# Kernel optimization log

Measured on AMD Instinct MI355X. Metric: run time of the kernel, lower is better.

## Reference

```python
import jax, jax.numpy as jnp
import numpy as np

B, N, D = 4, 4096, 512          # batch, seq_len, hidden_size
H, DH = 8, 64                    # n_heads, head_dim
M = 512                          # nb_features = 0.125 * seq_len
LN_EPS = 1e-12
KERNEL_EPS = 1e-4


def setup_inputs() -> dict:
    key = jax.random.key(0)
    ks = jax.random.split(key, 12)
    s = 0.02
    return {
        "input_tensor": jax.random.normal(ks[0], (B, N, D), jnp.float32),
        "attention_mask": jnp.zeros((B, 1, 1, N), jnp.float32),  # unused by module
        "Wq": jax.random.normal(ks[1], (D, D), jnp.float32) * s,
        "bq": jnp.zeros((D,), jnp.float32),
        "Wk": jax.random.normal(ks[2], (D, D), jnp.float32) * s,
        "bk": jnp.zeros((D,), jnp.float32),
        "Wv": jax.random.normal(ks[3], (D, D), jnp.float32) * s,
        "bv": jnp.zeros((D,), jnp.float32),
        # gaussian (orthogonal-style) random feature projections [M, DH]
        "proj_q": jax.random.normal(ks[4], (M, DH), jnp.float32),
        "proj_k": jax.random.normal(ks[5], (M, DH), jnp.float32),
        "Wd": jax.random.normal(ks[6], (D, D), jnp.float32) * s,
        "bd": jnp.zeros((D,), jnp.float32),
        "gamma": jnp.ones((D,), jnp.float32),
        "beta": jnp.zeros((D,), jnp.float32),
    }


def _softmax_kernel(data, projection_matrix, is_query):
    # data: [B,H,N,DH], projection_matrix: [M,DH]
    data_normalizer = data.shape[-1] ** (-0.25)
    ratio = projection_matrix.shape[0] ** (-0.5)
    data_dash = jnp.einsum("bhnd,md->bhnm", data_normalizer * data, projection_matrix)
    diag_data = (jnp.sum(data * data, axis=-1) * 0.5 * data_normalizer ** 2)[..., None]
    if is_query:
        stab = jnp.max(data_dash, axis=-1, keepdims=True)
    else:
        stab = jnp.max(data_dash)  # global max, per original code
    return ratio * (jnp.exp(data_dash - diag_data - stab) + KERNEL_EPS)


def _linear_attention(q, k, v):
    # q,k: [B,H,N,M]; v: [B,H,N,DH]
    k_cumsum = jnp.sum(k, axis=-2)                               # [B,H,M]
    d_inv = 1.0 / jnp.einsum("bhnm,bhm->bhn", q, k_cumsum)       # [B,H,N]
    context = jnp.einsum("bhnm,bhne->bhme", k, v)                # [B,H,M,DH]
    return jnp.einsum("bhme,bhnm,bhn->bhne", context, q, d_inv)  # [B,H,N,DH]


def reference(input_tensor, attention_mask, Wq, bq, Wk, bk, Wv, bv,
              proj_q, proj_k, Wd, bd, gamma, beta):
    def heads(x):  # [B,N,D] -> [B,H,N,DH]
        return x.reshape(B, N, H, DH).transpose(0, 2, 1, 3)

    q = heads(input_tensor @ Wq.T + bq)
    k = heads(input_tensor @ Wk.T + bk)
    v = heads(input_tensor @ Wv.T + bv)

    q = _softmax_kernel(q, proj_q, is_query=True)
    k = _softmax_kernel(k, proj_k, is_query=False)

    ctx = _linear_attention(q, k, v)                  # [B,H,N,DH]
    ctx = ctx.transpose(0, 2, 1, 3).reshape(B, N, D)  # merge heads

    hidden = ctx @ Wd.T + bd                          # dropout is identity (eval)
    x = hidden + input_tensor
    mu = jnp.mean(x, axis=-1, keepdims=True)
    var = jnp.mean((x - mu) ** 2, axis=-1, keepdims=True)
    return (x - mu) / jnp.sqrt(var + LN_EPS) * gamma + beta
```

## Files before the change

kernel.cpp:

```cpp
#include <hip/hip_runtime.h>
#include <math.h>

typedef __bf16 bf16;
typedef __bf16 bf16x8 __attribute__((ext_vector_type(8)));
typedef __bf16 bf16x4 __attribute__((ext_vector_type(4)));
typedef float  f32x4  __attribute__((ext_vector_type(4)));

#define NSEQ 4096
#define DMODEL 512
#define DHEAD 64
#define MFEAT 512
#define BHEADS 32
#define ROWS_TOTAL 16384

#define NORMALIZER 0.35355339059327373f
#define DIAG_C 0.0625f
#define KEPS 1e-4f

__device__ __forceinline__ float warpReduceSum(float v) {
#pragma unroll
    for (int off = 32; off > 0; off >>= 1) v += __shfl_xor(v, off);
    return v;
}

// ... 97 lines not shown
                int row = (wr << 6) + (mi << 4) + (l & 15);
                int addr = ((row << 7) + (ks << 6) + ((l >> 4) << 4)) ^ ((row & 7) << 4);
                af[mi] = *(const bf16x8*)(As + addr);
            }
#pragma unroll
            for (int nj = 0; nj < 4; ++nj) {
                int row = (wc << 6) + (nj << 4) + (l & 15);
                int addr = ((row << 7) + (ks << 6) + ((l >> 4) << 4)) ^ ((row & 7) << 4);
                bb[nj] = *(const bf16x8*)(Bs + addr);
            }
#pragma unroll
            for (int mi = 0; mi < 4; ++mi)
#pragma unroll
                for (int nj = 0; nj < 4; ++nj)
                    acc[mi][nj] = __builtin_amdgcn_mfma_f32_16x16x32_bf16(af[mi], bb[nj], acc[mi][nj], 0, 0, 0);
        }
        __syncthreads();
    }

    const int subrow = (l >> 4) << 2;
    const int subcol = l & 15;
#pragma unroll
    for (int mi = 0; mi < 4; ++mi) {
#pragma unroll
        for (int nj = 0; nj < 4; ++nj) {
            const int cg = col0 + (wc << 6) + (nj << 4) + subcol;
            const float bi = bias[cg];
            const int rgb = row0 + (wr << 6) + (mi << 4) + subrow;
            if (MODE == 0) {
                if (cg < 512) {
                    const int hh = cg >> 6, ee = cg & 63;
                    const int bb2 = rgb >> 12, n = rgb & 4095;
#pragma unroll
                    for (int r = 0; r < 4; ++r)
                        outQ[((size_t)((bb2 * 8 + hh) * 4096 + n + r)) * 64 + ee] =
                            (bf16)(acc[mi][nj][r] + bi);
                } else if (cg < 1024) {
                    const int eg = cg - 512, hh = eg >> 6, ee = eg & 63;
#pragma unroll
                    for (int r = 0; r < 4; ++r) {
                        const int rg = rgb + r;
                        *(bf16*)((char*)outK + (size_t)rg * 1024 + hh * 128 +
                                 ((ee * 2) ^ ((rg & 7) << 4))) = (bf16)(acc[mi][nj][r] + bi);
                    }
                } else {
                    const int eg = cg - 1024, hh = eg >> 6, ee = eg & 63;
                    const int bb2 = rgb >> 12, n = rgb & 4095;
                    bf16x4 pv;
#pragma unroll
                    for (int r = 0; r < 4; ++r) pv[r] = (bf16)(acc[mi][nj][r] + bi);
                    const int nb = n * 2;
                    size_t byteaddr = (size_t)((bb2 * 8 + hh) * 64 + ee) * 8192
                                    + (size_t)((nb & ~127) | ((nb & 127) ^ ((ee & 7) << 4)));
                    *(bf16x4*)((char*)outV + byteaddr) = pv;
                }
            } else {
#pragma unroll
                for (int r = 0; r < 4; ++r) {
                    const int rg = rgb + r;
                    outF[(size_t)rg * 512 + cg] = acc[mi][nj][r] + bi + resid[(size_t)rg * 512 + cg];
                }
            }
        }
    }
}

__global__ __launch_bounds__(64)
void vsum_kernel(const bf16* __restrict__ Vt, float* __restrict__ vsum)
{
    const int row = blockIdx.x;
    const bf16x8* p = (const bf16x8*)((const char*)Vt + (size_t)row * 8192);
    float s = 0.f;
#pragma unroll
    for (int i = 0; i < 8; ++i) {
        bf16x8 v = p[threadIdx.x + i * 64];
#pragma unroll
        for (int u = 0; u < 8; ++u) s += (float)v[u];
    }
    s = warpReduceSum(s);
    if (threadIdx.x == 0) vsum[row] = s;
}

__global__ __launch_bounds__(256)
void kside_mfma2(const bf16* __restrict__ Kb, const bf16* __restrict__ Vt,
                 const float* __restrict__ projk,
                 float* __restrict__ ctxp4, float* __restrict__ esumf4,
                 float* __restrict__ gmax)
{
    __shared__ char K_s[16384];
    __shared__ char V_s[16384];
    __shared__ char E_s[16384];
    __shared__ float diag_s[128];
    __shared__ float part_s[4][64];
    __shared__ float wmax_s[4];

    const int tid = threadIdx.x;
    const int w = tid >> 6, l = tid & 63;
    const int bh = blockIdx.x;
    const int b = bh >> 3, h = bh & 7;
    const int m0 = blockIdx.y << 6;
    const int z = blockIdx.z;

    bf16x8 pk[4][2];
#pragma unroll
    for (int nj = 0; nj < 4; ++nj)
#pragma unroll
        for (int ks = 0; ks < 2; ++ks) {
            const int m = m0 + (nj << 4) + (l & 15);
            const int e0 = (ks << 5) + ((l >> 4) << 3);
            const float* p = projk + (size_t)m * 64 + e0;
            float4 a = *(const float4*)p;
            float4 c = *(const float4*)(p + 4);
            bf16x8 f;
            f[0] = (bf16)a.x; f[1] = (bf16)a.y; f[2] = (bf16)a.z; f[3] = (bf16)a.w;
            f[4] = (bf16)c.x; f[5] = (bf16)c.y; f[6] = (bf16)c.z; f[7] = (bf16)c.w;
            pk[nj][ks] = f;
        }

    const char* kg = (const char*)Kb + ((size_t)(b * 4096) * 512 + h * 64) * 2
                   + (size_t)((w << 3) + (l >> 3)) * 1024 + ((l & 7) << 4);
    const char* vg = (const char*)Vt + (size_t)bh * 64 * 8192
                   + (size_t)((w << 2) + (l >> 4)) * 8192 + ((l & 15) << 4);

    float esacc[4] = {0.f, 0.f, 0.f, 0.f};
    float lmax = -1e30f;
    f32x4 acc2[4] = {};

    for (int c = 0; c < 8; ++c) {
        const int n0 = (z << 10) + (c << 7);
#pragma unroll
        for (int i = 0; i < 4; ++i) {
            gload16(kg + (size_t)(n0 + (i << 5)) * 1024, K_s + (i << 12) + (w << 10));
            gload16(vg + (size_t)(i << 4) * 8192 + (n0 << 1), V_s + (i << 12) + (w << 10));
        }
        __syncthreads();

        f32x4 acc1[2][4] = {};
        float ss[2] = {0.f, 0.f};
#pragma unroll
        for (int ks = 0; ks < 2; ++ks) {
            bf16x8 af[2];
#pragma unroll
            for (int mi = 0; mi < 2; ++mi) {
                const int n = (w << 5) + (mi << 4) + (l & 15);
                const int addr = ((n << 7) + (ks << 6) + ((l >> 4) << 4)) ^ ((n & 7) << 4);
                af[mi] = *(const bf16x8*)(K_s + addr);
#pragma unroll
                for (int u = 0; u < 8; ++u) { float f = (float)af[mi][u]; ss[mi] += f * f; }
            }
#pragma unroll
            for (int mi = 0; mi < 2; ++mi)
#pragma unroll
                for (int nj = 0; nj < 4; ++nj)
                    acc1[mi][nj] = __builtin_amdgcn_mfma_f32_16x16x32_bf16(af[mi], pk[nj][ks], acc1[mi][nj], 0, 0, 0);
        }
#pragma unroll
        for (int mi = 0; mi < 2; ++mi) {
            float s = ss[mi];
            s += __shfl_xor(s, 16); s += __shfl_xor(s, 32);
            if (l < 16) diag_s[(w << 5) + (mi << 4) + l] = DIAG_C * s;
        }
#pragma unroll
        for (int mi = 0; mi < 2; ++mi) {
            const int nrow0 = (w << 5) + (mi << 4) + ((l >> 4) << 2);
#pragma unroll
            for (int nj = 0; nj < 4; ++nj) {
                const int m = (nj << 4) + (l & 15);
                bf16x4 ev;
#pragma unroll
                for (int r = 0; r < 4; ++r) {
                    float kd = NORMALIZER * acc1[mi][nj][r];
                    lmax = fmaxf(lmax, kd);
                    float e = __expf(kd - diag_s[nrow0 + r]);
                    esacc[nj] += e;
                    ev[r] = (bf16)e;
                }
                const int addr = ((m << 8) + (nrow0 << 1)) ^ ((m & 7) << 4);
                *(bf16x4*)(E_s + addr) = ev;
            }
        }
        __syncthreads();

#pragma unroll
        for (int ks = 0; ks < 4; ++ks) {
            const int mrow = (w << 4) + (l & 15);
            const int aaddr = ((mrow << 8) + (ks << 6) + ((l >> 4) << 4)) ^ ((mrow & 7) << 4);
            bf16x8 aE = *(const bf16x8*)(E_s + aaddr);
#pragma unroll
            for (int ej = 0; ej < 4; ++ej) {
                const int e = (ej << 4) + (l & 15);
                const int vaddr = ((e << 8) + (ks << 6) + ((l >> 4) << 4)) ^ ((e & 7) << 4);
                bf16x8 bV = *(const bf16x8*)(V_s + vaddr);
                acc2[ej] = __builtin_amdgcn_mfma_f32_16x16x32_bf16(aE, bV, acc2[ej], 0, 0, 0);
            }
        }
        __syncthreads();
    }

#pragma unroll
    for (int nj = 0; nj < 4; ++nj) {
        float s = esacc[nj];
        s += __shfl_xor(s, 16); s += __shfl_xor(s, 32);
        if (l < 16) part_s[w][(nj << 4) + l] = s;
    }
#pragma unroll
    for (int off = 32; off > 0; off >>= 1) lmax = fmaxf(lmax, __shfl_xor(lmax, off));
    if (l == 0) wmax_s[w] = lmax;
    __syncthreads();
    if (tid < 64) {
        float es = part_s[0][tid] + part_s[1][tid] + part_s[2][tid] + part_s[3][tid];
        esumf4[((size_t)z * 32 + bh) * 512 + m0 + tid] = es;
        if (tid == 0)
            atomicMaxF(gmax, fmaxf(fmaxf(wmax_s[0], wmax_s[1]), fmaxf(wmax_s[2], wmax_s[3])));
    }
    const size_t zbase = (size_t)z * (32 * 512 * 64);
    const int mrow0 = m0 + (w << 4) + ((l >> 4) << 2);
#pragma unroll
    for (int ej = 0; ej < 4; ++ej) {
        const int e = (ej << 4) + (l & 15);
#pragma unroll
        for (int r = 0; r < 4; ++r)
            ctxp4[zbase + ((size_t)(bh * 512 + mrow0 + r)) * 64 + e] = acc2[ej][r];
    }
}

__global__ __launch_bounds__(256)
void finalize_ctx(const float* __restrict__ ctxp4, const float* __restrict__ esumf4,
                  bf16* __restrict__ ctxE, float* __restrict__ ctxsum,
                  float* __restrict__ esumsum)
{
    __shared__ float red_s[4][64];
    const int tid = threadIdx.x;
    const int bh = blockIdx.x;
    const int m0 = blockIdx.y << 7;
    const int e = tid & 63, ms = tid >> 6;
    const size_t Z = (size_t)32 * 512 * 64;

    const float* cb = ctxp4 + ((size_t)bh * 512 + m0 + ms * 32) * 64 + e;
    char* obr = (char*)ctxE + ((size_t)bh * 80 + e) * 1024;
    float s = 0.f;
#pragma unroll
    for (int i8 = 0; i8 < 4; ++i8) {
        bf16x8 pk8;
#pragma unroll
        for (int u = 0; u < 8; ++u) {
            const size_t off = (size_t)(i8 * 8 + u) * 64;
            float v = cb[off] + cb[off + Z] + cb[off + 2 * Z] + cb[off + 3 * Z];
            s += v;
            pk8[u] = (bf16)v;
        }
        const int inrow = ((m0 + ms * 32 + i8 * 8) << 1) ^ ((e & 7) << 4);
        *(bf16x8*)(obr + inrow) = pk8;
    }
    red_s[ms][e] = s;
    __syncthreads();
    if (tid < 64)
        atomicAdd(ctxsum + bh * 64 + tid,
                  red_s[0][tid] + red_s[1][tid] + red_s[2][tid] + red_s[3][tid]);
    if (tid < 128) {
        const int m = m0 + tid;
        float ev = esumf4[(size_t)bh * 512 + m]
                 + esumf4[((size_t)32 + bh) * 512 + m]
                 + esumf4[((size_t)64 + bh) * 512 + m]
                 + esumf4[((size_t)96 + bh) * 512 + m];
        bf16* er = ctxE + (size_t)(bh * 80 + 64) * 512;
        er[m] = (bf16)1.0f;
        er[512 + (m ^ 8)] = (bf16)ev;
        float t = warpReduceSum(ev);
        if ((tid & 63) == 0) atomicAdd(esumsum + bh, t);
    }
}

__global__ __launch_bounds__(512, 1)
void qside_mfma4(const bf16* __restrict__ Qb, const bf16* __restrict__ Pq,
                 const bf16* __restrict__ CtxE, const float* __restrict__ vsum,
                 const float* __restrict__ ctxsum, const float* __restrict__ esumsum,
                 const float* __restrict__ gmax, bf16* __restrict__ OutC)
{
    __shared__ char ctx_s[81920];
    __shared__ char pq_s[2][16384];
    __shared__ char T_s[40960];

    const int tid = threadIdx.x;
    const int w = tid >> 6, l = tid & 63;
    const int lq = l & 15, lg = l >> 4;
    const int bh = blockIdx.x;
    const int b = bh >> 3, h = bh & 7;
    const int n0 = blockIdx.y << 9;

    const char* ctxg = (const char*)CtxE + (size_t)bh * 81920;
    const char* pqg  = (const char*)Pq;
#pragma unroll
    for (int i = 0; i < 10; ++i)
        gload16(ctxg + (i << 13) + (tid << 4), ctx_s + (i << 13) + (w << 10));
#pragma unroll
    for (int p = 0; p < 2; ++p)
        gload16(pqg + (p << 13) + (tid << 4), pq_s[0] + (p << 13) + (w << 10));

    const char* qgb = (const char*)Qb + ((size_t)bh * 4096 + n0 + (w << 6)) * 128;
    bf16x8 qa[4][2];
    float diag_l[4];
#pragma unroll
    for (int ni = 0; ni < 4; ++ni) {
        const char* qr = qgb + ((ni << 4) + lq) * 128;
        float ss = 0.f;
#pragma unroll
        for (int kk = 0; kk < 2; ++kk) {
            qa[ni][kk] = *(const bf16x8*)(qr + (kk << 6) + (lg << 4));
#pragma unroll
            for (int u = 0; u < 8; ++u) { float f = (float)qa[ni][kk][u]; ss += f * f; }
        }
        ss += __shfl_xor(ss, 16);
        ss += __shfl_xor(ss, 32);
        diag_l[ni] = DIAG_C * ss;
    }

    f32x4 acc2[4][5] = {};
    float mmax[4] = {-1e30f, -1e30f, -1e30f, -1e30f};
    char* tw = T_s + w * 5120;
    const f32x4 Zc = {0.f, 0.f, 0.f, 0.f};

    __syncthreads();

    for (int ft = 0; ft < 4; ++ft) {
        const int buf = ft & 1;
        if (ft < 3) {
#pragma unroll
            for (int p = 0; p < 2; ++p)
                gload16(pqg + ((ft + 1) << 14) + (p << 13) + (tid << 4),
                        pq_s[buf ^ 1] + (p << 13) + (w << 10));
        }
        const char* pqb = pq_s[buf];
#pragma unroll
        for (int sl = 0; sl < 4; ++sl) {
            f32x4 acc1[2][4];
#pragma unroll
            for (int mi = 0; mi < 2; ++mi) {
                const int fr = (sl << 5) + (mi << 4) + lq;
                bf16x8 pf = *(const bf16x8*)(pqb + fr * 128 +
                              (((lg << 4)) ^ ((lq & 7) << 4)));
#pragma unroll
                for (int ni = 0; ni < 4; ++ni)
                    acc1[mi][ni] = __builtin_amdgcn_mfma_f32_16x16x32_bf16(pf, qa[ni][0], Zc, 0, 0, 0);
            }
#pragma unroll
            for (int mi = 0; mi < 2; ++mi) {
                const int fr = (sl << 5) + (mi << 4) + lq;
// ... 47 lines not shown
            const float uT = __shfl(acc2[ni][4][r], (lg << 4));
            const float uE = __shfl(acc2[ni][4][r], (lg << 4) | 1);
            const float cr = __expf(-NORMALIZER * mm);
            const float qsum = cr * uT + KEPS * 512.0f;
            const float D = sG * (cr * uE + KEPS * ess) + KEPS * 4096.0f * qsum;
            const float inv = 1.0f / D;
            const float al = sG * cr * inv;
            const float G1 = sG * KEPS * inv;
            const float G2 = KEPS * qsum * inv;
            const int row = (ni << 4) + (lg << 2) + r;
#pragma unroll
            for (int nj = 0; nj < 4; ++nj) {
                const int e = (nj << 4) + lq;
                float v = al * acc2[ni][nj][r] + G1 * ctxsum[(bh << 6) + e] + G2 * vsum[(bh << 6) + e];
                outb[(size_t)row * 512 + e] = (bf16)v;
            }
        }
    }
}

__global__ __launch_bounds__(256)
void ln_kernel(const float* __restrict__ hid, const float* __restrict__ gamma,
               const float* __restrict__ beta, float* __restrict__ out)
{
    const int row = (blockIdx.x << 2) + (threadIdx.x >> 6);
    const int lane = threadIdx.x & 63;
    const float* x = hid + (size_t)row * DMODEL + (lane << 3);
    float4 a = *(const float4*)x;
    float4 c = *(const float4*)(x + 4);
    float s = a.x + a.y + a.z + a.w + c.x + c.y + c.z + c.w;
    float sq = a.x * a.x + a.y * a.y + a.z * a.z + a.w * a.w +
               c.x * c.x + c.y * c.y + c.z * c.z + c.w * c.w;
    s = warpReduceSum(s);
    sq = warpReduceSum(sq);
    const float mu = s * 0.001953125f;
    const float var = sq * 0.001953125f - mu * mu;
    const float rs = rsqrtf(var + 1e-12f);
    const float4 g1 = *(const float4*)(gamma + (lane << 3));
    const float4 g2 = *(const float4*)(gamma + (lane << 3) + 4);
    const float4 b1 = *(const float4*)(beta + (lane << 3));
    const float4 b2 = *(const float4*)(beta + (lane << 3) + 4);
    float4 o1, o2;
    o1.x = (a.x - mu) * rs * g1.x + b1.x;
    o1.y = (a.y - mu) * rs * g1.y + b1.y;
    o1.z = (a.z - mu) * rs * g1.z + b1.z;
    o1.w = (a.w - mu) * rs * g1.w + b1.w;
    o2.x = (c.x - mu) * rs * g2.x + b2.x;
    o2.y = (c.y - mu) * rs * g2.y + b2.y;
    o2.z = (c.z - mu) * rs * g2.z + b2.z;
    o2.w = (c.w - mu) * rs * g2.w + b2.w;
    *(float4*)(out + (size_t)row * DMODEL + (lane << 3)) = o1;
    *(float4*)(out + (size_t)row * DMODEL + (lane << 3) + 4) = o2;
}

__global__ void init_misc(float* gmax)
{
    if (threadIdx.x == 0 && blockIdx.x == 0) *gmax = -1e30f;
}

extern "C" void kernel_launch(void* const* d_in, const int* in_sizes, int n_in,
                              void* d_out, int out_size, void* d_ws, size_t ws_size,
                              hipStream_t stream)
{
    const float* x     = (const float*)d_in[0];
    const float* Wq    = (const float*)d_in[2];
    const float* bq    = (const float*)d_in[3];
    const float* Wk    = (const float*)d_in[4];
    const float* bk    = (const float*)d_in[5];
    const float* Wv    = (const float*)d_in[6];
    const float* bv    = (const float*)d_in[7];
    const float* projq = (const float*)d_in[8];
    const float* projk = (const float*)d_in[9];
    const float* Wd    = (const float*)d_in[10];
    const float* bd    = (const float*)d_in[11];
    const float* gamma = (const float*)d_in[12];
    const float* beta  = (const float*)d_in[13];

    char* W = (char*)d_ws;
    bf16*  qb16   = (bf16*) (W);
    bf16*  kb16s  = (bf16*) (W + 16777216);
    bf16*  vtb    = (bf16*) (W + 33554432);
    bf16*  xb16   = (bf16*) (W + 50331648);
    float* hidf32 = (float*)(W + 67108864);
    float* ctxp4  = (float*)(W + 67108864);
    float* esumf4 = (float*)(W + 83886080);
    bf16*  Wb16   = (bf16*) (W + 100663296);
    bf16*  Wdb16  = (bf16*) (W + 102236160);
    bf16*  pqb16  = (bf16*) (W + 102760448);
    float* bcat   = (float*)(W + 102825984);
    bf16*  ctxE   = (bf16*) (W + 102832128);
    float* vsumb  = (float*)(W + 105453568);
    float* ctxsum = (float*)(W + 105461760);
    float* esmsm  = (float*)(W + 105469952);
    float* gmaxb  = (float*)(W + 105470080);

    prep_convert<<<9250, 256, 0, stream>>>(x, Wq, Wk, Wv, Wd, projq, bq, bk, bv,
                                           xb16, Wb16, Wdb16, pqb16, bcat);
    hipMemsetAsync(ctxE, 0, 2621440, stream);
    hipMemsetAsync(ctxsum, 0, 8192 + 128, stream);
    init_misc<<<1, 64, 0, stream>>>(gmaxb);

    gemm_mfma<0><<<dim3(12, 128), 256, 0, stream>>>(xb16, Wb16, bcat, nullptr,
                                                    qb16, kb16s, vtb, nullptr);

    vsum_kernel<<<2048, 64, 0, stream>>>(vtb, vsumb);
    kside_mfma2<<<dim3(32, 8, 4), 256, 0, stream>>>(kb16s, vtb, projk,
                                                    ctxp4, esumf4, gmaxb);
    finalize_ctx<<<dim3(32, 4), 256, 0, stream>>>(ctxp4, esumf4, ctxE, ctxsum, esmsm);

    qside_mfma4<<<dim3(32, 8), 512, 0, stream>>>(qb16, pqb16, ctxE, vsumb,
                                                 ctxsum, esmsm, gmaxb, xb16);

    gemm_mfma<1><<<dim3(4, 128), 256, 0, stream>>>(xb16, Wdb16, bd, x,
                                                   nullptr, nullptr, nullptr, hidf32);
    ln_kernel<<<4096, 256, 0, stream>>>(hidf32, gamma, beta, (float*)d_out);
}
```

Measured before the change: 193.6 us.

## Widen k-side feature tile to 128 and overlap K/V loads with compute

The k-side kernel now covers 128 random features per block instead of 64, so each K/V chunk loaded into shared memory feeds twice as many MFMAs and the grid's y-dimension halves. Diagonal norms are passed between lanes with shuffles instead of going through shared memory. The next K chunk is prefetched during the E·V MFMA phase and the V load is issued right after the barrier, which removes one barrier per iteration. In exchange the block uses more registers and more LDS (E_s is doubled) and launches fewer blocks, which may lower occupancy and parallelism.

```diff
diff --git a/kernel.cpp b/kernel.cpp
--- a/kernel.cpp
+++ b/kernel.cpp
@@ -203,146 +203,177 @@
 }
 
 __global__ __launch_bounds__(256)
-void kside_mfma2(const bf16* __restrict__ Kb, const bf16* __restrict__ Vt,
+void kside_mfma3(const bf16* __restrict__ Kb, const bf16* __restrict__ Vt,
                  const float* __restrict__ projk,
                  float* __restrict__ ctxp4, float* __restrict__ esumf4,
                  float* __restrict__ gmax)
 {
     __shared__ char K_s[16384];
     __shared__ char V_s[16384];
-    __shared__ char E_s[16384];
-    __shared__ float diag_s[128];
-    __shared__ float part_s[4][64];
+    __shared__ char E_s[32768];
+    __shared__ float part_s[4][128];
     __shared__ float wmax_s[4];
 
     const int tid = threadIdx.x;
     const int w = tid >> 6, l = tid & 63;
+    const int lq = l & 15, lg = l >> 4;
     const int bh = blockIdx.x;
     const int b = bh >> 3, h = bh & 7;
-    const int m0 = blockIdx.y << 6;
+    const int M0 = blockIdx.y << 7;
     const int z = blockIdx.z;
 
-    bf16x8 pk[4][2];
-#pragma unroll
-    for (int nj = 0; nj < 4; ++nj)
-#pragma unroll
-        for (int ks = 0; ks < 2; ++ks) {
-            const int m = m0 + (nj << 4) + (l & 15);
-            const int e0 = (ks << 5) + ((l >> 4) << 3);
-            const float* p = projk + (size_t)m * 64 + e0;
-            float4 a = *(const float4*)p;
-            float4 c = *(const float4*)(p + 4);
-            bf16x8 f;
-            f[0] = (bf16)a.x; f[1] = (bf16)a.y; f[2] = (bf16)a.z; f[3] = (bf16)a.w;
-            f[4] = (bf16)c.x; f[5] = (bf16)c.y; f[6] = (bf16)c.z; f[7] = (bf16)c.w;
-            pk[nj][ks] = f;
-        }
+    bf16x8 pk[2][4][2];
+#pragma unroll
+    for (int mh = 0; mh < 2; ++mh)
+#pragma unroll
+        for (int mj = 0; mj < 4; ++mj)
+#pragma unroll
+            for (int ks = 0; ks < 2; ++ks) {
+                const int m = M0 + (mh << 6) + (mj << 4) + lq;
+                const float* p = projk + (size_t)m * 64 + (ks << 5) + (lg << 3);
+                float4 a = *(const float4*)p;
+                float4 c = *(const float4*)(p + 4);
+                bf16x8 f;
+                f[0] = (bf16)a.x; f[1] = (bf16)a.y; f[2] = (bf16)a.z; f[3] = (bf16)a.w;
+                f[4] = (bf16)c.x; f[5] = (bf16)c.y; f[6] = (bf16)c.z; f[7] = (bf16)c.w;
+                pk[mh][mj][ks] = f;
+            }
 
     const char* kg = (const char*)Kb + ((size_t)(b * 4096) * 512 + h * 64) * 2
                    + (size_t)((w << 3) + (l >> 3)) * 1024 + ((l & 7) << 4);
     const char* vg = (const char*)Vt + (size_t)bh * 64 * 8192
                    + (size_t)((w << 2) + (l >> 4)) * 8192 + ((l & 15) << 4);
 
-    float esacc[4] = {0.f, 0.f, 0.f, 0.f};
+    float esacc[2][4] = {};
     float lmax = -1e30f;
-    f32x4 acc2[4] = {};
+    f32x4 acc2[2][4] = {};
+
+    {
+        const int n0 = z << 10;
+#pragma unroll
+        for (int i = 0; i < 4; ++i)
+            gload16(kg + (size_t)(n0 + (i << 5)) * 1024, K_s + (i << 12) + (w << 10));
+    }
 
     for (int c = 0; c < 8; ++c) {
-        const int n0 = (z << 10) + (c << 7);
-#pragma unroll
-        for (int i = 0; i < 4; ++i) {
-            gload16(kg + (size_t)(n0 + (i << 5)) * 1024, K_s + (i << 12) + (w << 10));
-            gload16(vg + (size_t)(i << 4) * 8192 + (n0 << 1), V_s + (i << 12) + (w << 10));
-        }
+        const int nc = (z << 10) + (c << 7);
         __syncthreads();
-
-        f32x4 acc1[2][4] = {};
+#pragma unroll
+        for (int i = 0; i < 4; ++i)
+            gload16(vg + (size_t)(i << 4) * 8192 + (nc << 1), V_s + (i << 12) + (w << 10));
+
+        bf16x8 af[2][2];
         float ss[2] = {0.f, 0.f};
 #pragma unroll
-        for (int ks = 0; ks < 2; ++ks) {
-            bf16x8 af[2];
-#pragma unroll
-            for (int mi = 0; mi < 2; ++mi) {
-                const int n = (w << 5) + (mi << 4) + (l & 15);
-                const int addr = ((n << 7) + (ks << 6) + ((l >> 4) << 4)) ^ ((n & 7) << 4);
-                af[mi] = *(const bf16x8*)(K_s + addr);
-#pragma unroll
-                for (int u = 0; u < 8; ++u) { float f = (float)af[mi][u]; ss[mi] += f * f; }
-            }
-#pragma unroll
-            for (int mi = 0; mi < 2; ++mi)
-#pragma unroll
-                for (int nj = 0; nj < 4; ++nj)
-                    acc1[mi][nj] = __builtin_amdgcn_mfma_f32_16x16x32_bf16(af[mi], pk[nj][ks], acc1[mi][nj], 0, 0, 0);
-        }
-#pragma unroll
-        for (int mi = 0; mi < 2; ++mi) {
-            float s = ss[mi];
+        for (int ni = 0; ni < 2; ++ni) {
+            const int n = (w << 5) + (ni << 4) + lq;
+#pragma unroll
+            for (int ks = 0; ks < 2; ++ks) {
+                const int addr = ((n << 7) + (ks << 6) + (lg << 4)) ^ ((n & 7) << 4);
+                af[ni][ks] = *(const bf16x8*)(K_s + addr);
+#pragma unroll
+                for (int u = 0; u < 8; ++u) { float f = (float)af[ni][ks][u]; ss[ni] += f * f; }
+            }
+            ss[ni] += __shfl_xor(ss[ni], 16);
+            ss[ni] += __shfl_xor(ss[ni], 32);
+        }
+        float dgc[2][4];
+#pragma unroll
+        for (int ni = 0; ni < 2; ++ni)
+#pragma unroll
+            for (int r = 0; r < 4; ++r)
+                dgc[ni][r] = DIAG_C * __shfl(ss[ni], (lg << 2) + r);
+
+#pragma unroll
+        for (int mh = 0; mh < 2; ++mh) {
+            f32x4 acc1[2][4] = {};
+#pragma unroll
+            for (int ks = 0; ks < 2; ++ks)
+#pragma unroll
+                for (int ni = 0; ni < 2; ++ni)
+#pragma unroll
+                    for (int mj = 0; mj < 4; ++mj)
+                        acc1[ni][mj] = __builtin_amdgcn_mfma_f32_16x16x32_bf16(
+                            af[ni][ks], pk[mh][mj][ks], acc1[ni][mj], 0, 0, 0);
+#pragma unroll
+            for (int ni = 0; ni < 2; ++ni) {
+                const int nl0 = (w << 5) + (ni << 4) + (lg << 2);
+#pragma unroll
+                for (int mj = 0; mj < 4; ++mj) {
+                    const int mloc = (mh << 6) + (mj << 4) + lq;
+                    bf16x4 ev;
+#pragma unroll
+                    for (int r = 0; r < 4; ++r) {
+                        float kd = NORMALIZER * acc1[ni][mj][r];
+                        lmax = fmaxf(lmax, kd);
+                        float e = __expf(kd - dgc[ni][r]);
+                        esacc[mh][mj] += e;
+                        ev[r] = (bf16)e;
+                    }
+                    const int addr = ((mloc << 8) + (nl0 << 1)) ^ ((mloc & 7) << 4);
+                    *(bf16x4*)(E_s + addr) = ev;
+                }
+            }
+        }
+        __syncthreads();
+        if (c < 7) {
+            const int nn = (z << 10) + ((c + 1) << 7);
+#pragma unroll
+            for (int i = 0; i < 4; ++i)
+                gload16(kg + (size_t)(nn + (i << 5)) * 1024, K_s + (i << 12) + (w << 10));
+        }
+#pragma unroll
+        for (int ks = 0; ks < 4; ++ks) {
+            bf16x8 ae[2];
+#pragma unroll
+            for (int mj2 = 0; mj2 < 2; ++mj2) {
+                const int mloc = (w << 5) + (mj2 << 4) + lq;
+                const int addr = ((mloc << 8) + (ks << 6) + (lg << 4)) ^ ((mloc & 7) << 4);
+                ae[mj2] = *(const bf16x8*)(E_s + addr);
+            }
+#pragma unroll
+            for (int ej = 0; ej < 4; ++ej) {
+                const int e = (ej << 4) + lq;
+                const int vaddr = ((e << 8) + (ks << 6) + (lg << 4)) ^ ((e & 7) << 4);
+                bf16x8 bV = *(const bf16x8*)(V_s + vaddr);
+#pragma unroll
+                for (int mj2 = 0; mj2 < 2; ++mj2)
+                    acc2[mj2][ej] = __builtin_amdgcn_mfma_f32_16x16x32_bf16(
+                        ae[mj2], bV, acc2[mj2][ej], 0, 0, 0);
+            }
+        }
+    }
+
+#pragma unroll
+    for (int mh = 0; mh < 2; ++mh)
+#pragma unroll
+        for (int mj = 0; mj < 4; ++mj) {
+            float s = esacc[mh][mj];
             s += __shfl_xor(s, 16); s += __shfl_xor(s, 32);
-            if (l < 16) diag_s[(w << 5) + (mi << 4) + l] = DIAG_C * s;
-        }
-#pragma unroll
-        for (int mi = 0; mi < 2; ++mi) {
-            const int nrow0 = (w << 5) + (mi << 4) + ((l >> 4) << 2);
-#pragma unroll
-            for (int nj = 0; nj < 4; ++nj) {
-                const int m = (nj << 4) + (l & 15);
-                bf16x4 ev;
-#pragma unroll
-                for (int r = 0; r < 4; ++r) {
-                    float kd = NORMALIZER * acc1[mi][nj][r];
-                    lmax = fmaxf(lmax, kd);
-                    float e = __expf(kd - diag_s[nrow0 + r]);
-                    esacc[nj] += e;
-                    ev[r] = (bf16)e;
-                }
-                const int addr = ((m << 8) + (nrow0 << 1)) ^ ((m & 7) << 4);
-                *(bf16x4*)(E_s + addr) = ev;
-            }
-        }
-        __syncthreads();
-
-#pragma unroll
-        for (int ks = 0; ks < 4; ++ks) {
-            const int mrow = (w << 4) + (l & 15);
-            const int aaddr = ((mrow << 8) + (ks << 6) + ((l >> 4) << 4)) ^ ((mrow & 7) << 4);
-            bf16x8 aE = *(const bf16x8*)(E_s + aaddr);
-#pragma unroll
-            for (int ej = 0; ej < 4; ++ej) {
-                const int e = (ej << 4) + (l & 15);
-                const int vaddr = ((e << 8) + (ks << 6) + ((l >> 4) << 4)) ^ ((e & 7) << 4);
-                bf16x8 bV = *(const bf16x8*)(V_s + vaddr);
-                acc2[ej] = __builtin_amdgcn_mfma_f32_16x16x32_bf16(aE, bV, acc2[ej], 0, 0, 0);
-            }
-        }
-        __syncthreads();
-    }
-
-#pragma unroll
-    for (int nj = 0; nj < 4; ++nj) {
-        float s = esacc[nj];
-        s += __shfl_xor(s, 16); s += __shfl_xor(s, 32);
-        if (l < 16) part_s[w][(nj << 4) + l] = s;
-    }
+            if (l < 16) part_s[w][(mh << 6) + (mj << 4) + l] = s;
+        }
 #pragma unroll
     for (int off = 32; off > 0; off >>= 1) lmax = fmaxf(lmax, __shfl_xor(lmax, off));
     if (l == 0) wmax_s[w] = lmax;
     __syncthreads();
-    if (tid < 64) {
+    if (tid < 128) {
         float es = part_s[0][tid] + part_s[1][tid] + part_s[2][tid] + part_s[3][tid];
-        esumf4[((size_t)z * 32 + bh) * 512 + m0 + tid] = es;
-        if (tid == 0)
-            atomicMaxF(gmax, fmaxf(fmaxf(wmax_s[0], wmax_s[1]), fmaxf(wmax_s[2], wmax_s[3])));
-    }
+        esumf4[((size_t)z * 32 + bh) * 512 + M0 + tid] = es;
+    }
+    if (tid == 0)
+        atomicMaxF(gmax, fmaxf(fmaxf(wmax_s[0], wmax_s[1]), fmaxf(wmax_s[2], wmax_s[3])));
     const size_t zbase = (size_t)z * (32 * 512 * 64);
-    const int mrow0 = m0 + (w << 4) + ((l >> 4) << 2);
-#pragma unroll
-    for (int ej = 0; ej < 4; ++ej) {
-        const int e = (ej << 4) + (l & 15);
-#pragma unroll
-        for (int r = 0; r < 4; ++r)
-            ctxp4[zbase + ((size_t)(bh * 512 + mrow0 + r)) * 64 + e] = acc2[ej][r];
-    }
+#pragma unroll
+    for (int mj2 = 0; mj2 < 2; ++mj2)
+#pragma unroll
+        for (int ej = 0; ej < 4; ++ej) {
+            const int e = (ej << 4) + lq;
+#pragma unroll
+            for (int r = 0; r < 4; ++r) {
+                const int mloc = (w << 5) + (mj2 << 4) + (lg << 2) + r;
+                ctxp4[zbase + ((size_t)(bh * 512 + M0 + mloc)) * 64 + e] = acc2[mj2][ej][r];
+            }
+        }
 }
 
 __global__ __launch_bounds__(256)
@@ -619,7 +650,7 @@
                                                     qb16, kb16s, vtb, nullptr);
 
     vsum_kernel<<<2048, 64, 0, stream>>>(vtb, vsumb);
-    kside_mfma2<<<dim3(32, 8, 4), 256, 0, stream>>>(kb16s, vtb, projk,
+    kside_mfma3<<<dim3(32, 4, 4), 256, 0, stream>>>(kb16s, vtb, projk,
                                                     ctxp4, esumf4, gmaxb);
     finalize_ctx<<<dim3(32, 4), 256, 0, stream>>>(ctxp4, esumf4, ctxE, ctxsum, esmsm);
 
```

New measurement: 197.3 us. Within noise of the previous version (+1.9%).

## Restructure K-side kernel to keep exp features in registers without LDS

Applied to the files above, without the earlier changes.

The K-side feature/context kernel is rewritten so each wave loads K and V fragments straight from global memory and builds the exp(K·P) tile in registers. A lane shuffle then reorders that tile into MFMA operand layout, replacing the LDS staging buffers and block barriers. The squared-norm diagonal term moves into a separate small kernel. Each block now covers 128 features and the sequence is split 8 ways instead of 4, with a transposed partial-context layout that finalize_ctx reads with vector loads. The aim is to cut synchronisation and LDS traffic and reduce how often K is reloaded, at the cost of an extra launch, more partial sums to reduce, and less coalesced global reads of V.

```diff
diff --git a/kernel.cpp b/kernel.cpp
--- a/kernel.cpp
+++ b/kernel.cpp
@@ -203,175 +203,183 @@
 }
 
 __global__ __launch_bounds__(256)
-void kside_mfma2(const bf16* __restrict__ Kb, const bf16* __restrict__ Vt,
-                 const float* __restrict__ projk,
-                 float* __restrict__ ctxp4, float* __restrict__ esumf4,
+void diag_kernel(const bf16* __restrict__ Kb, float* __restrict__ dgk)
+{
+    const int idx = blockIdx.x * 256 + threadIdx.x;
+    const int bh = idx >> 12, n = idx & 4095;
+    const int b = bh >> 3, h = bh & 7;
+    const char* row = (const char*)Kb + (size_t)(b * 4096 + n) * 1024 + h * 128;
+    const int sw = (n & 7) << 4;
+    float ss = 0.f;
+#pragma unroll
+    for (int j = 0; j < 8; ++j) {
+        bf16x8 v = *(const bf16x8*)(row + ((j << 4) ^ sw));
+#pragma unroll
+        for (int u = 0; u < 8; ++u) { float f = (float)v[u]; ss += f * f; }
+    }
+    dgk[idx] = DIAG_C * ss;
+}
+
+__global__ __launch_bounds__(256)
+void kside_mfma4(const bf16* __restrict__ Kb, const bf16* __restrict__ Vt,
+                 const float* __restrict__ projk, const float* __restrict__ dgk,
+                 float* __restrict__ ctxp8, float* __restrict__ esumf8,
                  float* __restrict__ gmax)
 {
-    __shared__ char K_s[16384];
-    __shared__ char V_s[16384];
-    __shared__ char E_s[16384];
-    __shared__ float diag_s[128];
-    __shared__ float part_s[4][64];
-    __shared__ float wmax_s[4];
-
     const int tid = threadIdx.x;
     const int w = tid >> 6, l = tid & 63;
+    const int lq = l & 15, lg = l >> 4;
     const int bh = blockIdx.x;
     const int b = bh >> 3, h = bh & 7;
-    const int m0 = blockIdx.y << 6;
+    const int M0w = (blockIdx.y << 7) + (w << 5);
     const int z = blockIdx.z;
-
-    bf16x8 pk[4][2];
-#pragma unroll
-    for (int nj = 0; nj < 4; ++nj)
+    const int nbase = z << 9;
+
+    bf16x8 pk[2][2];
+#pragma unroll
+    for (int mj = 0; mj < 2; ++mj)
 #pragma unroll
         for (int ks = 0; ks < 2; ++ks) {
-            const int m = m0 + (nj << 4) + (l & 15);
-            const int e0 = (ks << 5) + ((l >> 4) << 3);
-            const float* p = projk + (size_t)m * 64 + e0;
+            const int m = M0w + (mj << 4) + lq;
+            const float* p = projk + (size_t)m * 64 + (ks << 5) + (lg << 3);
             float4 a = *(const float4*)p;
             float4 c = *(const float4*)(p + 4);
             bf16x8 f;
             f[0] = (bf16)a.x; f[1] = (bf16)a.y; f[2] = (bf16)a.z; f[3] = (bf16)a.w;
             f[4] = (bf16)c.x; f[5] = (bf16)c.y; f[6] = (bf16)c.z; f[7] = (bf16)c.w;
-            pk[nj][ks] = f;
-        }
-
-    const char* kg = (const char*)Kb + ((size_t)(b * 4096) * 512 + h * 64) * 2
-                   + (size_t)((w << 3) + (l >> 3)) * 1024 + ((l & 7) << 4);
-    const char* vg = (const char*)Vt + (size_t)bh * 64 * 8192
-                   + (size_t)((w << 2) + (l >> 4)) * 8192 + ((l & 15) << 4);
-
-    float esacc[4] = {0.f, 0.f, 0.f, 0.f};
+            pk[mj][ks] = f;
+        }
+
+    const char* kgb = (const char*)Kb + (size_t)(b * 4096) * 1024 + h * 128;
+    const char* vgb = (const char*)Vt + (size_t)bh * 64 * 8192;
+    const float* dgb = dgk + bh * 4096;
+    const int swl = (lq & 7) << 4;
+
+    f32x4 acc2[4][2] = {};
+    float esacc[2] = {0.f, 0.f};
     float lmax = -1e30f;
-    f32x4 acc2[4] = {};
-
-    for (int c = 0; c < 8; ++c) {
-        const int n0 = (z << 10) + (c << 7);
-#pragma unroll
-        for (int i = 0; i < 4; ++i) {
-            gload16(kg + (size_t)(n0 + (i << 5)) * 1024, K_s + (i << 12) + (w << 10));
-            gload16(vg + (size_t)(i << 4) * 8192 + (n0 << 1), V_s + (i << 12) + (w << 10));
-        }
-        __syncthreads();
-
-        f32x4 acc1[2][4] = {};
-        float ss[2] = {0.f, 0.f};
-#pragma unroll
-        for (int ks = 0; ks < 2; ++ks) {
-            bf16x8 af[2];
-#pragma unroll
-            for (int mi = 0; mi < 2; ++mi) {
-                const int n = (w << 5) + (mi << 4) + (l & 15);
-                const int addr = ((n << 7) + (ks << 6) + ((l >> 4) << 4)) ^ ((n & 7) << 4);
-                af[mi] = *(const bf16x8*)(K_s + addr);
-#pragma unroll
-                for (int u = 0; u < 8; ++u) { float f = (float)af[mi][u]; ss[mi] += f * f; }
-            }
-#pragma unroll
-            for (int mi = 0; mi < 2; ++mi)
-#pragma unroll
-                for (int nj = 0; nj < 4; ++nj)
-                    acc1[mi][nj] = __builtin_amdgcn_mfma_f32_16x16x32_bf16(af[mi], pk[nj][ks], acc1[mi][nj], 0, 0, 0);
-        }
-#pragma unroll
-        for (int mi = 0; mi < 2; ++mi) {
-            float s = ss[mi];
-            s += __shfl_xor(s, 16); s += __shfl_xor(s, 32);
-            if (l < 16) diag_s[(w << 5) + (mi << 4) + l] = DIAG_C * s;
-        }
-#pragma unroll
-        for (int mi = 0; mi < 2; ++mi) {
-            const int nrow0 = (w << 5) + (mi << 4) + ((l >> 4) << 2);
-#pragma unroll
-            for (int nj = 0; nj < 4; ++nj) {
-                const int m = (nj << 4) + (l & 15);
-                bf16x4 ev;
+    const f32x4 Zc = {0.f, 0.f, 0.f, 0.f};
+
+    for (int c = 0; c < 4; ++c) {
+#pragma unroll
+        for (int g = 0; g < 4; ++g) {
+            const int nA = nbase + (c << 7) + (g << 5);
+            bf16x8 afA[2], afB[2];
+            {
+                const char* pA = kgb + (size_t)(nA + lq) * 1024;
+#pragma unroll
+                for (int ks = 0; ks < 2; ++ks) {
+                    const int off = ((ks << 6) + (lg << 4)) ^ swl;
+                    afA[ks] = *(const bf16x8*)(pA + off);
+                    afB[ks] = *(const bf16x8*)(pA + 16384 + off);
+                }
+            }
+            bf16x8 av[4];
+#pragma unroll
+            for (int et = 0; et < 4; ++et) {
+                const int e = (et << 4) + lq;
+                av[et] = *(const bf16x8*)(vgb + (size_t)e * 8192 +
+                           ((((nA + (lg << 3)) << 1)) ^ swl));
+            }
+            float4 dgA = *(const float4*)(dgb + nA + (lg << 2));
+            float4 dgB = *(const float4*)(dgb + nA + 16 + (lg << 2));
+            const float dgAr[4] = {dgA.x, dgA.y, dgA.z, dgA.w};
+            const float dgBr[4] = {dgB.x, dgB.y, dgB.z, dgB.w};
+            f32x4 dA[2], dB[2];
+#pragma unroll
+            for (int mj = 0; mj < 2; ++mj) {
+                dA[mj] = __builtin_amdgcn_mfma_f32_16x16x32_bf16(afA[0], pk[mj][0], Zc, 0, 0, 0);
+                dA[mj] = __builtin_amdgcn_mfma_f32_16x16x32_bf16(afA[1], pk[mj][1], dA[mj], 0, 0, 0);
+                dB[mj] = __builtin_amdgcn_mfma_f32_16x16x32_bf16(afB[0], pk[mj][0], Zc, 0, 0, 0);
+                dB[mj] = __builtin_amdgcn_mfma_f32_16x16x32_bf16(afB[1], pk[mj][1], dB[mj], 0, 0, 0);
+            }
+#pragma unroll
+            for (int mj = 0; mj < 2; ++mj) {
+                float eA[4], eB[4];
 #pragma unroll
                 for (int r = 0; r < 4; ++r) {
-                    float kd = NORMALIZER * acc1[mi][nj][r];
-                    lmax = fmaxf(lmax, kd);
-                    float e = __expf(kd - diag_s[nrow0 + r]);
-                    esacc[nj] += e;
-                    ev[r] = (bf16)e;
+                    const float kdA = NORMALIZER * dA[mj][r];
+                    const float kdB = NORMALIZER * dB[mj][r];
+                    lmax = fmaxf(lmax, fmaxf(kdA, kdB));
+                    eA[r] = __expf(kdA - dgAr[r]);
+                    eB[r] = __expf(kdB - dgBr[r]);
+                    esacc[mj] += eA[r] + eB[r];
                 }
-                const int addr = ((m << 8) + (nrow0 << 1)) ^ ((m & 7) << 4);
-                *(bf16x4*)(E_s + addr) = ev;
-            }
-        }
-        __syncthreads();
-
-#pragma unroll
-        for (int ks = 0; ks < 4; ++ks) {
-            const int mrow = (w << 4) + (l & 15);
-            const int aaddr = ((mrow << 8) + (ks << 6) + ((l >> 4) << 4)) ^ ((mrow & 7) << 4);
-            bf16x8 aE = *(const bf16x8*)(E_s + aaddr);
-#pragma unroll
-            for (int ej = 0; ej < 4; ++ej) {
-                const int e = (ej << 4) + (l & 15);
-                const int vaddr = ((e << 8) + (ks << 6) + ((l >> 4) << 4)) ^ ((e & 7) << 4);
-                bf16x8 bV = *(const bf16x8*)(V_s + vaddr);
-                acc2[ej] = __builtin_amdgcn_mfma_f32_16x16x32_bf16(aE, bV, acc2[ej], 0, 0, 0);
-            }
-        }
-        __syncthreads();
-    }
-
-#pragma unroll
-    for (int nj = 0; nj < 4; ++nj) {
-        float s = esacc[nj];
+                unsigned int wA0, wA1, wB0, wB1;
+                asm("v_cvt_pk_bf16_f32 %0, %1, %2" : "=v"(wA0) : "v"(eA[0]), "v"(eA[1]));
+                asm("v_cvt_pk_bf16_f32 %0, %1, %2" : "=v"(wA1) : "v"(eA[2]), "v"(eA[3]));
+                asm("v_cvt_pk_bf16_f32 %0, %1, %2" : "=v"(wB0) : "v"(eB[0]), "v"(eB[1]));
+                asm("v_cvt_pk_bf16_f32 %0, %1, %2" : "=v"(wB1) : "v"(eB[2]), "v"(eB[3]));
+                const int selE = (l >= 32) ? (int)wB0 : (int)wA0;
+                const int selO = (l >= 32) ? (int)wB1 : (int)wA1;
+                const int base = ((l & 16) << 1) + lq;
+                unsigned int w0 = (unsigned int)__shfl(selE, base);
+                unsigned int w1 = (unsigned int)__shfl(selO, base);
+                unsigned int w2 = (unsigned int)__shfl(selE, base + 16);
+                unsigned int w3 = (unsigned int)__shfl(selO, base + 16);
+                union { unsigned int u[4]; bf16x8 v; } bfr;
+                bfr.u[0] = w0; bfr.u[1] = w1; bfr.u[2] = w2; bfr.u[3] = w3;
+#pragma unroll
+                for (int et = 0; et < 4; ++et)
+                    acc2[et][mj] = __builtin_amdgcn_mfma_f32_16x16x32_bf16(
+                        av[et], bfr.v, acc2[et][mj], 0, 0, 0);
+            }
+        }
+    }
+
+#pragma unroll
+    for (int mj = 0; mj < 2; ++mj) {
+        float s = esacc[mj];
         s += __shfl_xor(s, 16); s += __shfl_xor(s, 32);
-        if (l < 16) part_s[w][(nj << 4) + l] = s;
+        if (l < 16)
+            esumf8[((size_t)z * 32 + bh) * 512 + M0w + (mj << 4) + lq] = s;
     }
 #pragma unroll
     for (int off = 32; off > 0; off >>= 1) lmax = fmaxf(lmax, __shfl_xor(lmax, off));
-    if (l == 0) wmax_s[w] = lmax;
-    __syncthreads();
-    if (tid < 64) {
-        float es = part_s[0][tid] + part_s[1][tid] + part_s[2][tid] + part_s[3][tid];
-        esumf4[((size_t)z * 32 + bh) * 512 + m0 + tid] = es;
-        if (tid == 0)
-            atomicMaxF(gmax, fmaxf(fmaxf(wmax_s[0], wmax_s[1]), fmaxf(wmax_s[2], wmax_s[3])));
-    }
-    const size_t zbase = (size_t)z * (32 * 512 * 64);
-    const int mrow0 = m0 + (w << 4) + ((l >> 4) << 2);
-#pragma unroll
-    for (int ej = 0; ej < 4; ++ej) {
-        const int e = (ej << 4) + (l & 15);
-#pragma unroll
-        for (int r = 0; r < 4; ++r)
-            ctxp4[zbase + ((size_t)(bh * 512 + mrow0 + r)) * 64 + e] = acc2[ej][r];
-    }
+    if (l == 0) atomicMaxF(gmax, lmax);
+
+    float* cz = ctxp8 + (size_t)z * (32 * 64 * 512) + (size_t)bh * 64 * 512;
+#pragma unroll
+    for (int et = 0; et < 4; ++et)
+#pragma unroll
+        for (int mj = 0; mj < 2; ++mj)
+#pragma unroll
+            for (int r = 0; r < 4; ++r) {
+                const int e = (et << 4) + (lg << 2) + r;
+                cz[(size_t)e * 512 + M0w + (mj << 4) + lq] = acc2[et][mj][r];
+            }
 }
 
 __global__ __launch_bounds__(256)
-void finalize_ctx(const float* __restrict__ ctxp4, const float* __restrict__ esumf4,
+void finalize_ctx(const float* __restrict__ ctxp8, const float* __restrict__ esumf8,
                   bf16* __restrict__ ctxE, float* __restrict__ ctxsum,
                   float* __restrict__ esumsum)
 {
     __shared__ float red_s[4][64];
     const int tid = threadIdx.x;
     const int bh = blockIdx.x;
-    const int m0 = blockIdx.y << 7;
+    const int mc = blockIdx.y << 7;
     const int e = tid & 63, ms = tid >> 6;
-    const size_t Z = (size_t)32 * 512 * 64;
-
-    const float* cb = ctxp4 + ((size_t)bh * 512 + m0 + ms * 32) * 64 + e;
+    const size_t Z = (size_t)32 * 64 * 512;
+
+    const float* cb = ctxp8 + (size_t)bh * 64 * 512 + (size_t)e * 512 + mc + (ms << 5);
     char* obr = (char*)ctxE + ((size_t)bh * 80 + e) * 1024;
     float s = 0.f;
 #pragma unroll
     for (int i8 = 0; i8 < 4; ++i8) {
-        bf16x8 pk8;
-#pragma unroll
-        for (int u = 0; u < 8; ++u) {
-            const size_t off = (size_t)(i8 * 8 + u) * 64;
-            float v = cb[off] + cb[off + Z] + cb[off + 2 * Z] + cb[off + 3 * Z];
-            s += v;
-            pk8[u] = (bf16)v;
-        }
-        const int inrow = ((m0 + ms * 32 + i8 * 8) << 1) ^ ((e & 7) << 4);
-        *(bf16x8*)(obr + inrow) = pk8;
+        float acc[8] = {};
+#pragma unroll
+        for (int zz = 0; zz < 8; ++zz) {
+            float4 v0 = *(const float4*)(cb + zz * Z + (i8 << 3));
+            float4 v1 = *(const float4*)(cb + zz * Z + (i8 << 3) + 4);
+            acc[0] += v0.x; acc[1] += v0.y; acc[2] += v0.z; acc[3] += v0.w;
+            acc[4] += v1.x; acc[5] += v1.y; acc[6] += v1.z; acc[7] += v1.w;
+        }
+        bf16x8 p8;
+#pragma unroll
+        for (int u = 0; u < 8; ++u) { s += acc[u]; p8[u] = (bf16)acc[u]; }
+        const int mloc = mc + (ms << 5) + (i8 << 3);
+        *(bf16x8*)(obr + ((mloc << 1) ^ ((e & 7) << 4))) = p8;
     }
     red_s[ms][e] = s;
     __syncthreads();
@@ -379,11 +387,11 @@
         atomicAdd(ctxsum + bh * 64 + tid,
                   red_s[0][tid] + red_s[1][tid] + red_s[2][tid] + red_s[3][tid]);
     if (tid < 128) {
-        const int m = m0 + tid;
-        float ev = esumf4[(size_t)bh * 512 + m]
-                 + esumf4[((size_t)32 + bh) * 512 + m]
-                 + esumf4[((size_t)64 + bh) * 512 + m]
-                 + esumf4[((size_t)96 + bh) * 512 + m];
+        const int m = mc + tid;
+        float ev = 0.f;
+#pragma unroll
+        for (int zz = 0; zz < 8; ++zz)
+            ev += esumf8[((size_t)zz * 32 + bh) * 512 + m];
         bf16* er = ctxE + (size_t)(bh * 80 + 64) * 512;
         er[m] = (bf16)1.0f;
         er[512 + (m ^ 8)] = (bf16)ev;
@@ -597,8 +605,9 @@
     bf16*  vtb    = (bf16*) (W + 33554432);
     bf16*  xb16   = (bf16*) (W + 50331648);
     float* hidf32 = (float*)(W + 67108864);
-    float* ctxp4  = (float*)(W + 67108864);
-    float* esumf4 = (float*)(W + 83886080);
+    float* ctxp8  = (float*)(W + 67108864);
+    float* esumf8 = (float*)(W + 100663296);
+    float* dgk    = (float*)(W + 101187584);
     bf16*  Wb16   = (bf16*) (W + 100663296);
     bf16*  Wdb16  = (bf16*) (W + 102236160);
     bf16*  pqb16  = (bf16*) (W + 102760448);
@@ -618,10 +627,11 @@
     gemm_mfma<0><<<dim3(12, 128), 256, 0, stream>>>(xb16, Wb16, bcat, nullptr,
                                                     qb16, kb16s, vtb, nullptr);
 
+    diag_kernel<<<512, 256, 0, stream>>>(kb16s, dgk);
     vsum_kernel<<<2048, 64, 0, stream>>>(vtb, vsumb);
-    kside_mfma2<<<dim3(32, 8, 4), 256, 0, stream>>>(kb16s, vtb, projk,
-                                                    ctxp4, esumf4, gmaxb);
-    finalize_ctx<<<dim3(32, 4), 256, 0, stream>>>(ctxp4, esumf4, ctxE, ctxsum, esmsm);
+    kside_mfma4<<<dim3(32, 4, 8), 256, 0, stream>>>(kb16s, vtb, projk, dgk,
+                                                    ctxp8, esumf8, gmaxb);
+    finalize_ctx<<<dim3(32, 4), 256, 0, stream>>>(ctxp8, esumf8, ctxE, ctxsum, esmsm);
 
     qside_mfma4<<<dim3(32, 8), 512, 0, stream>>>(qb16, pqb16, ctxE, vsumb,
                                                  ctxsum, esmsm, gmaxb, xb16);
```

Result: slower. 218.5 us (+12.9%).

## Precompute K row norms and read K/V fragments directly from global memory

Applied to the files above, without the earlier changes.

The K-side kernel no longer stages K and V tiles into shared memory. MFMA operands are loaded straight from global memory, relying on the existing swizzled storage layout. The per-row squared-norm term is moved into a separate diag_kernel that writes to a workspace buffer, so the main loop no longer reduces it itself. This removes LDS staging and one barrier per chunk, at the cost of an extra launch, extra global traffic and possibly less coalesced per-lane global loads.

```diff
diff --git a/kernel.cpp b/kernel.cpp
--- a/kernel.cpp
+++ b/kernel.cpp
@@ -203,20 +203,36 @@
 }
 
 __global__ __launch_bounds__(256)
-void kside_mfma2(const bf16* __restrict__ Kb, const bf16* __restrict__ Vt,
-                 const float* __restrict__ projk,
+void diag_kernel(const bf16* __restrict__ Kb, float* __restrict__ dgk)
+{
+    const int idx = blockIdx.x * 256 + threadIdx.x;
+    const int bh = idx >> 12, n = idx & 4095;
+    const int b = bh >> 3, h = bh & 7;
+    const char* row = (const char*)Kb + (size_t)(b * 4096 + n) * 1024 + h * 128;
+    const int sw = (n & 7) << 4;
+    float ss = 0.f;
+#pragma unroll
+    for (int j = 0; j < 8; ++j) {
+        bf16x8 v = *(const bf16x8*)(row + ((j << 4) ^ sw));
+#pragma unroll
+        for (int u = 0; u < 8; ++u) { float f = (float)v[u]; ss += f * f; }
+    }
+    dgk[idx] = DIAG_C * ss;
+}
+
+__global__ __launch_bounds__(256)
+void kside_mfma5(const bf16* __restrict__ Kb, const bf16* __restrict__ Vt,
+                 const float* __restrict__ projk, const float* __restrict__ dgk,
                  float* __restrict__ ctxp4, float* __restrict__ esumf4,
                  float* __restrict__ gmax)
 {
-    __shared__ char K_s[16384];
-    __shared__ char V_s[16384];
     __shared__ char E_s[16384];
-    __shared__ float diag_s[128];
     __shared__ float part_s[4][64];
     __shared__ float wmax_s[4];
 
     const int tid = threadIdx.x;
     const int w = tid >> 6, l = tid & 63;
+    const int lq = l & 15, lg = l >> 4;
     const int bh = blockIdx.x;
     const int b = bh >> 3, h = bh & 7;
     const int m0 = blockIdx.y << 6;
@@ -224,79 +240,71 @@
 
     bf16x8 pk[4][2];
 #pragma unroll
-    for (int nj = 0; nj < 4; ++nj)
+    for (int mj = 0; mj < 4; ++mj)
 #pragma unroll
         for (int ks = 0; ks < 2; ++ks) {
-            const int m = m0 + (nj << 4) + (l & 15);
-            const int e0 = (ks << 5) + ((l >> 4) << 3);
-            const float* p = projk + (size_t)m * 64 + e0;
+            const int m = m0 + (mj << 4) + lq;
+            const float* p = projk + (size_t)m * 64 + (ks << 5) + (lg << 3);
             float4 a = *(const float4*)p;
             float4 c = *(const float4*)(p + 4);
             bf16x8 f;
             f[0] = (bf16)a.x; f[1] = (bf16)a.y; f[2] = (bf16)a.z; f[3] = (bf16)a.w;
             f[4] = (bf16)c.x; f[5] = (bf16)c.y; f[6] = (bf16)c.z; f[7] = (bf16)c.w;
-            pk[nj][ks] = f;
-        }
-
-    const char* kg = (const char*)Kb + ((size_t)(b * 4096) * 512 + h * 64) * 2
-                   + (size_t)((w << 3) + (l >> 3)) * 1024 + ((l & 7) << 4);
-    const char* vg = (const char*)Vt + (size_t)bh * 64 * 8192
-                   + (size_t)((w << 2) + (l >> 4)) * 8192 + ((l & 15) << 4);
+            pk[mj][ks] = f;
+        }
+
+    const char* kgb = (const char*)Kb + (size_t)(b * 4096) * 1024 + h * 128;
+    const char* vgb = (const char*)Vt + (size_t)bh * 64 * 8192;
+    const float* dgb = dgk + (bh << 12) + (z << 10);
+    const int swl = (lq & 7) << 4;
 
     float esacc[4] = {0.f, 0.f, 0.f, 0.f};
     float lmax = -1e30f;
     f32x4 acc2[4] = {};
+    const f32x4 Zc = {0.f, 0.f, 0.f, 0.f};
 
     for (int c = 0; c < 8; ++c) {
-        const int n0 = (z << 10) + (c << 7);
-#pragma unroll
-        for (int i = 0; i < 4; ++i) {
-            gload16(kg + (size_t)(n0 + (i << 5)) * 1024, K_s + (i << 12) + (w << 10));
-            gload16(vg + (size_t)(i << 4) * 8192 + (n0 << 1), V_s + (i << 12) + (w << 10));
-        }
-        __syncthreads();
-
-        f32x4 acc1[2][4] = {};
-        float ss[2] = {0.f, 0.f};
-#pragma unroll
-        for (int ks = 0; ks < 2; ++ks) {
-            bf16x8 af[2];
-#pragma unroll
-            for (int mi = 0; mi < 2; ++mi) {
-                const int n = (w << 5) + (mi << 4) + (l & 15);
-                const int addr = ((n << 7) + (ks << 6) + ((l >> 4) << 4)) ^ ((n & 7) << 4);
-                af[mi] = *(const bf16x8*)(K_s + addr);
-#pragma unroll
-                for (int u = 0; u < 8; ++u) { float f = (float)af[mi][u]; ss[mi] += f * f; }
-            }
-#pragma unroll
-            for (int mi = 0; mi < 2; ++mi)
-#pragma unroll
-                for (int nj = 0; nj < 4; ++nj)
-                    acc1[mi][nj] = __builtin_amdgcn_mfma_f32_16x16x32_bf16(af[mi], pk[nj][ks], acc1[mi][nj], 0, 0, 0);
-        }
-#pragma unroll
-        for (int mi = 0; mi < 2; ++mi) {
-            float s = ss[mi];
-            s += __shfl_xor(s, 16); s += __shfl_xor(s, 32);
-            if (l < 16) diag_s[(w << 5) + (mi << 4) + l] = DIAG_C * s;
-        }
-#pragma unroll
-        for (int mi = 0; mi < 2; ++mi) {
-            const int nrow0 = (w << 5) + (mi << 4) + ((l >> 4) << 2);
-#pragma unroll
-            for (int nj = 0; nj < 4; ++nj) {
-                const int m = (nj << 4) + (l & 15);
+        const int nc = (z << 10) + (c << 7);
+        const int nw = nc + (w << 5);
+
+        bf16x8 af[2][2];
+#pragma unroll
+        for (int ni = 0; ni < 2; ++ni) {
+            const char* pA = kgb + (size_t)(nw + (ni << 4) + lq) * 1024;
+#pragma unroll
+            for (int ks = 0; ks < 2; ++ks)
+                af[ni][ks] = *(const bf16x8*)(pA + (((ks << 6) + (lg << 4)) ^ swl));
+        }
+        f32x4 acc1[2][4];
+#pragma unroll
+        for (int ni = 0; ni < 2; ++ni)
+#pragma unroll
+            for (int mj = 0; mj < 4; ++mj) {
+                acc1[ni][mj] = __builtin_amdgcn_mfma_f32_16x16x32_bf16(af[ni][0], pk[mj][0], Zc, 0, 0, 0);
+                acc1[ni][mj] = __builtin_amdgcn_mfma_f32_16x16x32_bf16(af[ni][1], pk[mj][1], acc1[ni][mj], 0, 0, 0);
+            }
+        float dgr[2][4];
+#pragma unroll
+        for (int ni = 0; ni < 2; ++ni) {
+            float4 dv = *(const float4*)(dgb + (c << 7) + (w << 5) + (ni << 4) + (lg << 2));
+            dgr[ni][0] = dv.x; dgr[ni][1] = dv.y; dgr[ni][2] = dv.z; dgr[ni][3] = dv.w;
+        }
+#pragma unroll
+        for (int ni = 0; ni < 2; ++ni) {
+            const int nl = (w << 5) + (ni << 4) + (lg << 2);
+#pragma unroll
+            for (int mj = 0; mj < 4; ++mj) {
+                const int m = (mj << 4) + lq;
                 bf16x4 ev;
 #pragma unroll
                 for (int r = 0; r < 4; ++r) {
-                    float kd = NORMALIZER * acc1[mi][nj][r];
+                    float kd = NORMALIZER * acc1[ni][mj][r];
                     lmax = fmaxf(lmax, kd);
-                    float e = __expf(kd - diag_s[nrow0 + r]);
-                    esacc[nj] += e;
+                    float e = __expf(kd - dgr[ni][r]);
+                    esacc[mj] += e;
                     ev[r] = (bf16)e;
                 }
-                const int addr = ((m << 8) + (nrow0 << 1)) ^ ((m & 7) << 4);
+                const int addr = ((m << 8) + (nl << 1)) ^ ((m & 7) << 4);
                 *(bf16x4*)(E_s + addr) = ev;
             }
         }
@@ -304,14 +312,14 @@
 
 #pragma unroll
         for (int ks = 0; ks < 4; ++ks) {
-            const int mrow = (w << 4) + (l & 15);
-            const int aaddr = ((mrow << 8) + (ks << 6) + ((l >> 4) << 4)) ^ ((mrow & 7) << 4);
+            const int mrow = (w << 4) + lq;
+            const int aaddr = ((mrow << 8) + (ks << 6) + (lg << 4)) ^ ((mrow & 7) << 4);
             bf16x8 aE = *(const bf16x8*)(E_s + aaddr);
 #pragma unroll
             for (int ej = 0; ej < 4; ++ej) {
-                const int e = (ej << 4) + (l & 15);
-                const int vaddr = ((e << 8) + (ks << 6) + ((l >> 4) << 4)) ^ ((e & 7) << 4);
-                bf16x8 bV = *(const bf16x8*)(V_s + vaddr);
+                const int e = (ej << 4) + lq;
+                bf16x8 bV = *(const bf16x8*)(vgb + (size_t)e * 8192 +
+                              ((((nc + (ks << 5) + (lg << 3)) << 1)) ^ swl));
                 acc2[ej] = __builtin_amdgcn_mfma_f32_16x16x32_bf16(aE, bV, acc2[ej], 0, 0, 0);
             }
         }
@@ -319,10 +327,10 @@
     }
 
 #pragma unroll
-    for (int nj = 0; nj < 4; ++nj) {
-        float s = esacc[nj];
+    for (int mj = 0; mj < 4; ++mj) {
+        float s = esacc[mj];
         s += __shfl_xor(s, 16); s += __shfl_xor(s, 32);
-        if (l < 16) part_s[w][(nj << 4) + l] = s;
+        if (l < 16) part_s[w][(mj << 4) + l] = s;
     }
 #pragma unroll
     for (int off = 32; off > 0; off >>= 1) lmax = fmaxf(lmax, __shfl_xor(lmax, off));
@@ -335,10 +343,10 @@
             atomicMaxF(gmax, fmaxf(fmaxf(wmax_s[0], wmax_s[1]), fmaxf(wmax_s[2], wmax_s[3])));
     }
     const size_t zbase = (size_t)z * (32 * 512 * 64);
-    const int mrow0 = m0 + (w << 4) + ((l >> 4) << 2);
+    const int mrow0 = m0 + (w << 4) + (lg << 2);
 #pragma unroll
     for (int ej = 0; ej < 4; ++ej) {
-        const int e = (ej << 4) + (l & 15);
+        const int e = (ej << 4) + lq;
 #pragma unroll
         for (int r = 0; r < 4; ++r)
             ctxp4[zbase + ((size_t)(bh * 512 + mrow0 + r)) * 64 + e] = acc2[ej][r];
@@ -599,6 +607,7 @@
     float* hidf32 = (float*)(W + 67108864);
     float* ctxp4  = (float*)(W + 67108864);
     float* esumf4 = (float*)(W + 83886080);
+    float* dgk    = (float*)(W + 84148224);
     bf16*  Wb16   = (bf16*) (W + 100663296);
     bf16*  Wdb16  = (bf16*) (W + 102236160);
     bf16*  pqb16  = (bf16*) (W + 102760448);
@@ -618,8 +627,9 @@
     gemm_mfma<0><<<dim3(12, 128), 256, 0, stream>>>(xb16, Wb16, bcat, nullptr,
                                                     qb16, kb16s, vtb, nullptr);
 
+    diag_kernel<<<512, 256, 0, stream>>>(kb16s, dgk);
     vsum_kernel<<<2048, 64, 0, stream>>>(vtb, vsumb);
-    kside_mfma2<<<dim3(32, 8, 4), 256, 0, stream>>>(kb16s, vtb, projk,
+    kside_mfma5<<<dim3(32, 8, 4), 256, 0, stream>>>(kb16s, vtb, projk, dgk,
                                                     ctxp4, esumf4, gmaxb);
     finalize_ctx<<<dim3(32, 4), 256, 0, stream>>>(ctxp4, esumf4, ctxE, ctxsum, esmsm);
 
```

Result: slower. 225.8 us (+16.7%).
